# Kernel optimization log

Measured on AMD Instinct MI355X. Metric: run time of the kernel, lower is better.

The kernel has to match this reference:

```python
import jax, jax.numpy as jnp
import numpy as np

DIM = 512
HEADS = 8
DIM_HEAD = 64
INNER = HEADS * DIM_HEAD          # 512
GROUPS = 8                        # offset_groups
OFF_D = INNER // GROUPS           # 64
DS = 4                            # downsample_factor
KS = 6                            # offset_kernel_size
OFF_SCALE = 4.0                   # offset_scale (defaults to downsample_factor)
SCALE = DIM_HEAD ** -0.5


def conv1d(x, w, b=None, stride=1, padding=0, groups=1):
    # x: (B, Cin, N), w: (Cout, Cin//groups, K)
    out = jax.lax.conv_general_dilated(
        x, w, (stride,), [(padding, padding)],
        dimension_numbers=('NCH', 'OIH', 'NCH'), feature_group_count=groups)
    if b is not None:
        out = out + b[None, :, None]
    return out


def grid_sample_1d(feats, grid):
    # Faithful to F.grid_sample(mode='bilinear', padding_mode='zeros', align_corners=False)
    # applied along a length-N axis (the 2D workaround's width dim is size 1 -> identity).
    # feats: (B, C, N), grid: (B, M) normalized coords.
    N = feats.shape[-1]
    pos = ((grid + 1.0) * N - 1.0) * 0.5          # unnormalize, align_corners=False
    x0 = jnp.floor(pos)
    w1 = (pos - x0)[:, None, :]                    # fractional weight, (B,1,M)

    def gather(idx):
        valid = ((idx >= 0) & (idx < N))[:, None, :]
        idxc = jnp.clip(idx, 0, N - 1).astype(jnp.int32)
        g = jnp.take_along_axis(feats, idxc[:, None, :], axis=2)  # (B,C,M)
        return g * valid

    return gather(x0) * (1.0 - w1) + gather(x0 + 1.0) * w1


def setup_inputs() -> dict:
    key = jax.random.key(0)
    ks = jax.random.split(key, 10)
    n = 4096
    x = jax.random.normal(ks[0], (1, n, DIM), dtype=jnp.float32)
    prev_x = jax.random.normal(ks[1], (1, n, DIM), dtype=jnp.float32)

    def w(k, shape, fan_in):
        return jax.random.normal(k, shape, dtype=jnp.float32) * (fan_in ** -0.5)

    Wq = w(ks[2], (INNER, 2 * DIM // GROUPS, 1), 2 * DIM // GROUPS)   # grouped 1x1
    Wk = w(ks[3], (INNER, DIM // GROUPS, 1), DIM // GROUPS)
    Wv = w(ks[4], (INNER, DIM // GROUPS, 1), DIM // GROUPS)
    Wo = w(ks[5], (DIM, INNER, 1), INNER)
    bo = jnp.zeros((DIM,), dtype=jnp.float32)
    Woff_dw = w(ks[6], (OFF_D, 1, KS), KS)                             # depthwise
    boff_dw = jnp.zeros((OFF_D,), dtype=jnp.float32)
    Woff_p = w(ks[7], (1, OFF_D, 1), OFF_D)                            # to 1 channel
    return {"x": x, "prev_x": prev_x, "Wq": Wq, "Wk": Wk, "Wv": Wv,
            "Wo": Wo, "bo": bo, "Woff_dw": Woff_dw, "boff_dw": boff_dw,
            "Woff_p": Woff_p}


def reference(x, prev_x, Wq, Wk, Wv, Wo, bo, Woff_dw, boff_dw, Woff_p):
    b = x.shape[0]                    # must be 1 (module's einsum relies on broadcast)
    x_t = jnp.swapaxes(x, 1, 2)       # (b, dim, n)
    px_t = jnp.swapaxes(prev_x, 1, 2)
    n = x_t.shape[-1]

    cq = jnp.concatenate([px_t, x_t], axis=1)          # (b, 2*dim, n)
    q = conv1d(cq, Wq, groups=GROUPS)                  # (b, inner, n)

    # offset network on grouped queries
    gq = q.reshape(b * GROUPS, OFF_D, n)
    h = conv1d(gq, Woff_dw, boff_dw, stride=DS, padding=(KS - DS) // 2, groups=OFF_D)
    h = jax.nn.gelu(h, approximate=False)
    off = conv1d(h, Woff_p)[:, 0, :]                   # (b*g, m)
    off = jnp.tanh(off) * OFF_SCALE
    m = off.shape[-1]                                  # n // DS

    vgrid = jnp.arange(m, dtype=off.dtype) + off       # (b*g, m)
    vgrid = 2.0 * vgrid / max(m - 1, 1) - 1.0          # normalize_grid
    vgrid = jnp.tile(vgrid, (2, 1))                    # (2*b*g, m)

    kv_in = jnp.concatenate([px_t, x_t], axis=0)       # (2b, dim, n)
    gkv = kv_in.reshape(2 * b * GROUPS, OFF_D, n)
    kv = grid_sample_1d(gkv, vgrid)                    # (2bg, off_d, m)
    kv = kv.reshape(2 * b, INNER, m)

    k = conv1d(kv, Wk, groups=GROUPS)                  # (2b, inner, m)
    v = conv1d(kv, Wv, groups=GROUPS)

    qh = (q * SCALE).reshape(b, HEADS, DIM_HEAD, n).transpose(0, 1, 3, 2)   # (b,h,n,d)
    kh = k.reshape(2 * b, HEADS, DIM_HEAD, m).transpose(0, 1, 3, 2)         # (2b,h,m,d)
    vh = v.reshape(2 * b, HEADS, DIM_HEAD, m).transpose(0, 1, 3, 2)

    qh = jnp.broadcast_to(qh, (2 * b,) + qh.shape[1:])  # explicit torch-einsum broadcast
    sim = jnp.einsum('bhid,bhjd->bhij', qh, kh)         # (2b,h,n,m)
    attn = jax.nn.softmax(sim, axis=-1)
    out = jnp.einsum('bhij,bhjd->bhid', attn, vh)       # (2b,h,n,d)

    out = out.transpose(0, 1, 3, 2).reshape(2 * b, INNER, n)
    out = conv1d(out, Wo, bo)                           # (2b, dim, n)
    out = jnp.swapaxes(out, 1, 2)                       # (2b, n, dim)
    out = out.reshape(2, b, n, DIM)
    return out.mean(axis=0)                             # (b, n, dim) -- avg prev/cur streams
```

## Files before the change

kernel.cpp:

```cpp
#include <hip/hip_runtime.h>
#include <math.h>

#define DIMC 512
#define NG 8
#define QSCALE 0.18033688011112042f
#define MSHIFT 7.2134752044448170f

typedef _Float16 half8 __attribute__((ext_vector_type(8)));
typedef __fp16 fp16x2 __attribute__((ext_vector_type(2)));
typedef float f32x4 __attribute__((ext_vector_type(4)));

__device__ __forceinline__ half8 frag_f32(const float* p) {
    float4 a = *(const float4*)p;
    float4 b = *(const float4*)(p + 4);
    union { fp16x2 h2[4]; half8 h8; } u;
    u.h2[0] = __builtin_amdgcn_cvt_pkrtz(a.x, a.y);
    u.h2[1] = __builtin_amdgcn_cvt_pkrtz(a.z, a.w);
    u.h2[2] = __builtin_amdgcn_cvt_pkrtz(b.x, b.y);
    u.h2[3] = __builtin_amdgcn_cvt_pkrtz(b.z, b.w);
    return u.h8;
}

__global__ __launch_bounds__(256, 2) void k_front(
    const float* __restrict__ x, const float* __restrict__ px,
    const float* __restrict__ Wq, const float* __restrict__ Wk,
    const float* __restrict__ Wv, const float* __restrict__ Wo,
    const float* __restrict__ Wdw, const float* __restrict__ bdw,
    const float* __restrict__ Wp, _Float16* __restrict__ qh,
    _Float16* __restrict__ kt16, _Float16* __restrict__ vt16,
    _Float16* __restrict__ Woh, int n, int m)
{
    __shared__ float Os[64*69];
    __shared__ float hl[2][64];
    __shared__ float part[16][16];
    __shared__ int   x0s[16];
    __shared__ float w1s[16];
    __shared__ _Float16 kvs[2][16*72];
    int g  = blockIdx.x & 7;
    int jt = blockIdx.x >> 3;
    int P0 = jt*64, j0 = jt*16;
    int t  = threadIdx.x;
    int lane = t & 63, w = t >> 6;
    int l15 = lane & 15, quad = lane >> 4;
    const float* SRC = (g < 4) ? px : x;
    int cbase = (g & 3) * 128;

    if (blockIdx.x < 128) {
        int idx = blockIdx.x*2048 + t*8;
        float4 a = *(const float4*)&Wo[idx];
        float4 b = *(const float4*)&Wo[idx+4];
        union { fp16x2 h2[4]; uint4 v; } pk;
        pk.h2[0] = __builtin_amdgcn_cvt_pkrtz(a.x, a.y);
        pk.h2[1] = __builtin_amdgcn_cvt_pkrtz(a.z, a.w);
        pk.h2[2] = __builtin_amdgcn_cvt_pkrtz(b.x, b.y);
        pk.h2[3] = __builtin_amdgcn_cvt_pkrtz(b.z, b.w);
        *(uint4*)&Woh[idx] = pk.v;
    }

    if (t < 128) {
        int side = t >> 6, c = t & 63;
        int p = P0 + (side ? 64 : -1);
        float hsum = 0.f;
        if (p >= 0 && p < n) {
            const float* xr = &SRC[(size_t)p*DIMC + cbase];
            const float* wr = &Wq[(size_t)(g*64 + c)*128];
#pragma unroll 8
            for (int k = 0; k < 32; ++k) {
                float4 xv = *(const float4*)&xr[k*4];
                float4 wv = *(const float4*)&wr[k*4];
                hsum += xv.x*wv.x + xv.y*wv.y + xv.z*wv.z + xv.w*wv.w;
            }
        }
        hl[side][c] = hsum;
    }

    half8 af[4];
#pragma unroll
    for (int ks = 0; ks < 4; ++ks)
        af[ks] = frag_f32(&SRC[(size_t)(P0 + w*16 + l15)*DIMC + cbase + ks*32 + quad*8]);
    f32x4 acc[4];
#pragma unroll
    for (int nt = 0; nt < 4; ++nt) acc[nt] = (f32x4){0.f,0.f,0.f,0.f};
#pragma unroll
    for (int ks = 0; ks < 4; ++ks)
#pragma unroll
        for (int nt = 0; nt < 4; ++nt) {
            half8 bf = frag_f32(&Wq[(size_t)(g*64 + nt*16 + l15)*128 + ks*32 + quad*8]);
            acc[nt] = __builtin_amdgcn_mfma_f32_16x16x32_f16(af[ks], bf, acc[nt], 0, 0, 0);
        }
#pragma unroll
    for (int nt = 0; nt < 4; ++nt)
#pragma unroll
        for (int r = 0; r < 4; ++r)
            Os[(w*16 + quad*4 + r)*69 + nt*16 + l15] = acc[nt][r];
    __syncthreads();

    {
        int i = t >> 2, hf = t & 3;
        union { _Float16 h[16]; uint4 v[2]; } pk;
#pragma unroll
        for (int u = 0; u < 16; ++u) pk.h[u] = (_Float16)(Os[i*69 + hf*16 + u] * QSCALE);
        uint4* dst = (uint4*)&qh[((size_t)g*n + P0 + i)*64 + hf*16];
        dst[0] = pk.v[0]; dst[1] = pk.v[1];
    }

    {
        int j = t & 15, cg = t >> 4;
        float acco = 0.f;
#pragma unroll
        for (int cc = 0; cc < 4; ++cc) {
            int c = cg*4 + cc;
            float h = bdw[c];
#pragma unroll
            for (int tt = 0; tt < 6; ++tt) {
                int lp = 4*j + tt - 1;
                float val = (lp < 0) ? hl[0][c] : (lp >= 64 ? hl[1][c] : Os[lp*69 + c]);
                h += Wdw[c*6 + tt] * val;
            }
            float ge = 0.5f * h * (1.0f + erff(h * 0.70710678118654752f));
            acco += Wp[c] * ge;
        }
        part[cg][j] = acco;
    }
    __syncthreads();
    if (t < 16) {
        float off = 0.f;
#pragma unroll
        for (int cg2 = 0; cg2 < 16; ++cg2) off += part[cg2][t];
        off = tanhf(off) * 4.0f;
        int jg = j0 + t;
        float vg  = 2.0f * ((float)jg + off) / (float)(m - 1) - 1.0f;
        float pos = ((vg + 1.0f) * (float)n - 1.0f) * 0.5f;
        float x0  = floorf(pos);
        x0s[t] = (int)x0;
        w1s[t] = pos - x0;
    }
    __syncthreads();

    {
        float a0[4], a1[4], b0[4], b1[4], wg[4];
#pragma unroll
        for (int jj = 0; jj < 4; ++jj) {
            int j = jj*4 + w;
            int ii = x0s[j];
            wg[jj] = w1s[j];
            bool v0 = (ii   >= 0 && ii   < n);
            bool v1 = (ii+1 >= 0 && ii+1 < n);
            a0[jj] = v0 ? px[(size_t)ii*DIMC + g*64 + lane]     : 0.f;
            a1[jj] = v1 ? px[(size_t)(ii+1)*DIMC + g*64 + lane] : 0.f;
            b0[jj] = v0 ? x[(size_t)ii*DIMC + g*64 + lane]      : 0.f;
            b1[jj] = v1 ? x[(size_t)(ii+1)*DIMC + g*64 + lane]  : 0.f;
        }
#pragma unroll
        for (int jj = 0; jj < 4; ++jj) {
            kvs[0][(jj*4 + w)*72 + lane] = (_Float16)(a0[jj]*(1.0f - wg[jj]) + a1[jj]*wg[jj]);
            kvs[1][(jj*4 + w)*72 + lane] = (_Float16)(b0[jj]*(1.0f - wg[jj]) + b1[jj]*wg[jj]);
        }
    }
    __syncthreads();

    half8 bk[2], bv[2];
#pragma unroll
    for (int ks = 0; ks < 2; ++ks) {
        bk[ks] = frag_f32(&Wk[(size_t)(g*64 + w*16 + l15)*64 + ks*32 + quad*8]);
        bv[ks] = frag_f32(&Wv[(size_t)(g*64 + w*16 + l15)*64 + ks*32 + quad*8]);
    }
#pragma unroll
    for (int s = 0; s < 2; ++s) {
        half8 afk[2];
#pragma unroll
        for (int ks = 0; ks < 2; ++ks)
            afk[ks] = *(const half8*)&kvs[s][l15*72 + ks*32 + quad*8];
        f32x4 ack = (f32x4){0.f,0.f,0.f,0.f};
        f32x4 acv = (f32x4){0.f,0.f,0.f,0.f};
#pragma unroll
        for (int ks = 0; ks < 2; ++ks) {
            ack = __builtin_amdgcn_mfma_f32_16x16x32_f16(afk[ks], bk[ks], ack, 0, 0, 0);
            acv = __builtin_amdgcn_mfma_f32_16x16x32_f16(afk[ks], bv[ks], acv, 0, 0, 0);
        }
        size_t hb = (size_t)(s*8 + g);
#pragma unroll
        for (int r = 0; r < 4; ++r)
            kt16[(hb*m + j0 + quad*4 + r)*64 + w*16 + l15] = (_Float16)ack[r];
        union { fp16x2 h2[2]; uint2 v; } pv;
        pv.h2[0] = __builtin_amdgcn_cvt_pkrtz(acv[0], acv[1]);
        pv.h2[1] = __builtin_amdgcn_cvt_pkrtz(acv[2], acv[3]);
        *(uint2*)&vt16[(hb*64 + w*16 + l15)*m + j0 + quad*4] = pv.v;
    }
}

__global__ __launch_bounds__(256, 2) void k_attn(
    const _Float16* __restrict__ qh, const _Float16* __restrict__ kt16,
    const _Float16* __restrict__ vt16, _Float16* __restrict__ aoh, int n, int m)
{
    __shared__ _Float16 Vs[2][64*72];
    __shared__ _Float16 Ps[128*72];
    int nit = n >> 7;
    int it = blockIdx.x % nit;
    int h  = (blockIdx.x / nit) & 7;
    int s  = blockIdx.x / (nit*8);
    int t  = threadIdx.x;
    int lane = t & 63, w = t >> 6;
    int l15 = lane & 15, quad = lane >> 4;
    int i0 = it*128;

    const _Float16* qb = &qh[((size_t)h*n + i0)*64];
    half8 bqv[2][2];
#pragma unroll
    for (int ks = 0; ks < 2; ++ks)
#pragma unroll
        for (int i2 = 0; i2 < 2; ++i2)
            bqv[ks][i2] = *(const half8*)&qb[(w*32 + i2*16 + l15)*64 + ks*32 + quad*8];

    const _Float16* kb = &kt16[(size_t)(s*8+h)*m*64];
    const _Float16* vb = &vt16[(size_t)(s*8+h)*64*m];

    int r0 = t >> 3, oct = t & 7;

    float lsum[2] = {0.f, 0.f};
    f32x4 oaccT[4][2];
#pragma unroll
    for (int dt = 0; dt < 4; ++dt)
#pragma unroll
        for (int i2 = 0; i2 < 2; ++i2) oaccT[dt][i2] = (f32x4){0.f,0.f,0.f,0.f};

    uint4 pv0 = *(const uint4*)&vb[(size_t)r0*m + oct*8];
    uint4 pv1 = *(const uint4*)&vb[(size_t)(r0+32)*m + oct*8];
    *(uint4*)&Vs[0][r0*72 + oct*8]      = pv0;
    *(uint4*)&Vs[0][(r0+32)*72 + oct*8] = pv1;

    int ntile = m >> 6;
    for (int tk = 0; tk < ntile; ++tk) {
        bool pf = (tk + 1 < ntile);
        if (pf) {
            pv0 = *(const uint4*)&vb[(size_t)r0*m + (tk+1)*64 + oct*8];
            pv1 = *(const uint4*)&vb[(size_t)(r0+32)*m + (tk+1)*64 + oct*8];
        }
        half8 aqv[2][4];
#pragma unroll
        for (int ks = 0; ks < 2; ++ks)
#pragma unroll
            for (int jt = 0; jt < 4; ++jt)
                aqv[ks][jt] = *(const half8*)&kb[(size_t)(tk*64 + jt*16 + l15)*64 + ks*32 + quad*8];

        __syncthreads();
        const _Float16* VB = Vs[tk & 1];
        half8 avv[2][4];
#pragma unroll
        for (int ks = 0; ks < 2; ++ks)
#pragma unroll
            for (int dt = 0; dt < 4; ++dt)
                avv[ks][dt] = *(const half8*)&VB[(dt*16 + l15)*72 + ks*32 + quad*8];

        f32x4 accs[4][2];
#pragma unroll
        for (int jt = 0; jt < 4; ++jt)
#pragma unroll
            for (int i2 = 0; i2 < 2; ++i2) accs[jt][i2] = (f32x4){0.f,0.f,0.f,0.f};
        __builtin_amdgcn_s_setprio(1);
#pragma unroll
        for (int ks = 0; ks < 2; ++ks)
#pragma unroll
            for (int jt = 0; jt < 4; ++jt)
#pragma unroll
                for (int i2 = 0; i2 < 2; ++i2)
                    accs[jt][i2] = __builtin_amdgcn_mfma_f32_16x16x32_f16(
                        aqv[ks][jt], bqv[ks][i2], accs[jt][i2], 0, 0, 0);
        __builtin_amdgcn_s_setprio(0);

#pragma unroll
        for (int jt = 0; jt < 4; ++jt)
#pragma unroll
            for (int i2 = 0; i2 < 2; ++i2) {
                f32x4 p;
#pragma unroll
                for (int r = 0; r < 4; ++r) p[r] = __builtin_amdgcn_exp2f(accs[jt][i2][r] - MSHIFT);
                lsum[i2] += (p[0]+p[1]) + (p[2]+p[3]);
                union { fp16x2 h; int i; } c0, c1;
                c0.h = __builtin_amdgcn_cvt_pkrtz(p[0], p[1]);
                c1.h = __builtin_amdgcn_cvt_pkrtz(p[2], p[3]);
                *(int2*)&Ps[(w*32 + i2*16 + l15)*72 + jt*16 + quad*4] = make_int2(c0.i, c1.i);
            }

        __builtin_amdgcn_s_setprio(1);
#pragma unroll
        for (int ks = 0; ks < 2; ++ks)
#pragma unroll
            for (int i2 = 0; i2 < 2; ++i2) {
                half8 bp = *(const half8*)&Ps[(w*32 + i2*16 + l15)*72 + ks*32 + quad*8];
#pragma unroll
                for (int dt = 0; dt < 4; ++dt)
                    oaccT[dt][i2] = __builtin_amdgcn_mfma_f32_16x16x32_f16(
                        avv[ks][dt], bp, oaccT[dt][i2], 0, 0, 0);
            }
        __builtin_amdgcn_s_setprio(0);

        if (pf) {
            int b2 = (tk + 1) & 1;
            *(uint4*)&Vs[b2][r0*72 + oct*8]      = pv0;
            *(uint4*)&Vs[b2][(r0+32)*72 + oct*8] = pv1;
        }
    }

#pragma unroll
    for (int i2 = 0; i2 < 2; ++i2) {
        lsum[i2] += __shfl_xor(lsum[i2], 16, 64);
        lsum[i2] += __shfl_xor(lsum[i2], 32, 64);
    }
    float inv[2] = {1.0f / lsum[0], 1.0f / lsum[1]};
#pragma unroll
    for (int dt = 0; dt < 4; ++dt)
#pragma unroll
        for (int i2 = 0; i2 < 2; ++i2)
#pragma unroll
            for (int r = 0; r < 4; ++r)
                Ps[(w*32 + i2*16 + l15)*72 + dt*16 + quad*4 + r]
                    = (_Float16)(oaccT[dt][i2][r] * inv[i2]);
    {
        int row = w*32 + (lane >> 1);
        int dbase = (lane & 1) * 32;
        size_t gbase = (size_t)(i0 + row)*1024 + s*512 + h*64 + dbase;
#pragma unroll
        for (int k2 = 0; k2 < 4; ++k2) {
            uint4 v = *(uint4*)&Ps[row*72 + dbase + k2*8];
            *(uint4*)&aoh[gbase + k2*8] = v;
        }
    }
}

__global__ __launch_bounds__(256) void k_out(
    const _Float16* __restrict__ aoh, const _Float16* __restrict__ Woh,
    const float* __restrict__ bo, float* __restrict__ out, int n)
{
    int i0 = blockIdx.x*64, d0 = blockIdx.y*64;
    int t = threadIdx.x;
    int lane = t & 63, w = t >> 6;
    int l15 = lane & 15, quad = lane >> 4;
    f32x4 oacc[4];
#pragma unroll
    for (int dt = 0; dt < 4; ++dt) oacc[dt] = (f32x4){0.f,0.f,0.f,0.f};

    const _Float16* arow = &aoh[(size_t)(i0 + w*16 + l15)*1024 + quad*8];
#pragma unroll 4
    for (int ks = 0; ks < 16; ++ks) {
        half8 aq0 = *(const half8*)&arow[ks*32];
        half8 aq1 = *(const half8*)&arow[(ks+16)*32];
        half8 aqs = aq0 + aq1;
        int cbase = ks * 32;
#pragma unroll
        for (int dt = 0; dt < 4; ++dt) {
            half8 bw = *(const half8*)&Woh[(size_t)(d0 + dt*16 + l15)*DIMC + cbase + quad*8];
            oacc[dt] = __builtin_amdgcn_mfma_f32_16x16x32_f16(aqs, bw, oacc[dt], 0, 0, 0);
        }
    }
#pragma unroll
    for (int dt = 0; dt < 4; ++dt) {
        float bias = bo[d0 + dt*16 + l15];
#pragma unroll
        for (int r = 0; r < 4; ++r)
            out[(size_t)(i0 + w*16 + quad*4 + r)*DIMC + d0 + dt*16 + l15]
                = bias + 0.5f*oacc[dt][r];
    }
}

extern "C" void kernel_launch(void* const* d_in, const int* in_sizes, int n_in,
                              void* d_out, int out_size, void* d_ws, size_t ws_size,
                              hipStream_t stream)
{
    const float* x   = (const float*)d_in[0];
    const float* px  = (const float*)d_in[1];
    const float* Wq  = (const float*)d_in[2];
    const float* Wk  = (const float*)d_in[3];
    const float* Wv  = (const float*)d_in[4];
    const float* Wo  = (const float*)d_in[5];
    const float* bo  = (const float*)d_in[6];
    const float* Wdw = (const float*)d_in[7];
    const float* bdw = (const float*)d_in[8];
    const float* Wp  = (const float*)d_in[9];
    float* out = (float*)d_out;
    int n = in_sizes[0] / DIMC;
    int m = n / 4;

    _Float16* qhf  = (_Float16*)d_ws;
    _Float16* kt16 = qhf + (size_t)8*n*64;
    _Float16* vt16 = kt16 + (size_t)16*m*64;
    _Float16* aoh  = vt16 + (size_t)16*m*64;
    _Float16* Woh  = aoh + (size_t)n*1024;

    k_front<<<8*(m/16),    256, 0, stream>>>(x, px, Wq, Wk, Wv, Wo, Wdw, bdw, Wp,
                                             qhf, kt16, vt16, Woh, n, m);
    k_attn <<<2*8*(n/128), 256, 0, stream>>>(qhf, kt16, vt16, aoh, n, m);
    k_out  <<<dim3(n/64, 8), 256, 0, stream>>>(aoh, Woh, bo, out, n);
}
```

Measured before the change: 158.1 us.

## Load V fragments directly from global into registers, drop shared-memory staging

The attention kernel no longer stages V tiles through a double-buffered shared-memory array with a per-tile __syncthreads. Each wave now loads its V MFMA fragments straight from global memory into registers, ping-ponging two register sets across an unrolled-by-two loop so the next tile's load overlaps the current tile's compute. This removes the block barrier and the shared-memory round trip. In exchange it raises register pressure, and the global reads are strided by m per row instead of being issued cooperatively and coalesced. Each wave also re-reads the full V tile rather than sharing one copy.

Result: slower. 185.0 us (+17.0%).

```diff
diff --git a/kernel.cpp b/kernel.cpp
--- a/kernel.cpp
+++ b/kernel.cpp
@@ -189,11 +189,83 @@
     }
 }
 
+struct AttnCtx {
+    const _Float16* kb;
+    const _Float16* vb;
+    _Float16* Ps;
+    int m, w, l15, quad;
+};
+
+__device__ __forceinline__ void load_v(const AttnCtx& c, half8 (&dst)[2][4], int tk) {
+#pragma unroll
+    for (int ks = 0; ks < 2; ++ks)
+#pragma unroll
+        for (int dt = 0; dt < 4; ++dt)
+            dst[ks][dt] = *(const half8*)&c.vb[(size_t)(dt*16 + c.l15)*c.m
+                                              + tk*64 + ks*32 + c.quad*8];
+}
+
+__device__ __forceinline__ void attn_body(
+    const AttnCtx& c, int tk, const half8 (&avv)[2][4],
+    const half8 (&bqv)[2][2], float (&lsum)[2], f32x4 (&oaccT)[4][2])
+{
+    half8 aqv[2][4];
+#pragma unroll
+    for (int ks = 0; ks < 2; ++ks)
+#pragma unroll
+        for (int jt = 0; jt < 4; ++jt)
+            aqv[ks][jt] = *(const half8*)&c.kb[(size_t)(tk*64 + jt*16 + c.l15)*64
+                                              + ks*32 + c.quad*8];
+
+    f32x4 accs[4][2];
+#pragma unroll
+    for (int jt = 0; jt < 4; ++jt)
+#pragma unroll
+        for (int i2 = 0; i2 < 2; ++i2) accs[jt][i2] = (f32x4){0.f,0.f,0.f,0.f};
+    __builtin_amdgcn_s_setprio(1);
+#pragma unroll
+    for (int ks = 0; ks < 2; ++ks)
+#pragma unroll
+        for (int jt = 0; jt < 4; ++jt)
+#pragma unroll
+            for (int i2 = 0; i2 < 2; ++i2)
+                accs[jt][i2] = __builtin_amdgcn_mfma_f32_16x16x32_f16(
+                    aqv[ks][jt], bqv[ks][i2], accs[jt][i2], 0, 0, 0);
+    __builtin_amdgcn_s_setprio(0);
+
+#pragma unroll
+    for (int jt = 0; jt < 4; ++jt)
+#pragma unroll
+        for (int i2 = 0; i2 < 2; ++i2) {
+            f32x4 p;
+#pragma unroll
+            for (int r = 0; r < 4; ++r) p[r] = __builtin_amdgcn_exp2f(accs[jt][i2][r] - MSHIFT);
+            lsum[i2] += (p[0]+p[1]) + (p[2]+p[3]);
+            union { fp16x2 h; int i; } c0, c1;
+            c0.h = __builtin_amdgcn_cvt_pkrtz(p[0], p[1]);
+            c1.h = __builtin_amdgcn_cvt_pkrtz(p[2], p[3]);
+            *(int2*)&c.Ps[(c.w*32 + i2*16 + c.l15)*72 + jt*16 + c.quad*4]
+                = make_int2(c0.i, c1.i);
+        }
+
+    __builtin_amdgcn_s_setprio(1);
+#pragma unroll
+    for (int ks = 0; ks < 2; ++ks)
+#pragma unroll
+        for (int i2 = 0; i2 < 2; ++i2) {
+            half8 bp = *(const half8*)&c.Ps[(c.w*32 + i2*16 + c.l15)*72 + ks*32 + c.quad*8];
+#pragma unroll
+            for (int dt = 0; dt < 4; ++dt)
+                oaccT[dt][i2] = __builtin_amdgcn_mfma_f32_16x16x32_f16(
+                    avv[ks][dt], bp, oaccT[dt][i2], 0, 0, 0);
+        }
+    __builtin_amdgcn_s_setprio(0);
+}
+
 __global__ __launch_bounds__(256, 2) void k_attn(
     const _Float16* __restrict__ qh, const _Float16* __restrict__ kt16,
     const _Float16* __restrict__ vt16, _Float16* __restrict__ aoh, int n, int m)
 {
-    __shared__ _Float16 Vs[2][64*72];
     __shared__ _Float16 Ps[128*72];
     int nit = n >> 7;
     int it = blockIdx.x % nit;
@@ -212,10 +284,10 @@
         for (int i2 = 0; i2 < 2; ++i2)
             bqv[ks][i2] = *(const half8*)&qb[(w*32 + i2*16 + l15)*64 + ks*32 + quad*8];
 
-    const _Float16* kb = &kt16[(size_t)(s*8+h)*m*64];
-    const _Float16* vb = &vt16[(size_t)(s*8+h)*64*m];
-
-    int r0 = t >> 3, oct = t & 7;
+    AttnCtx c;
+    c.kb = &kt16[(size_t)(s*8+h)*m*64];
+    c.vb = &vt16[(size_t)(s*8+h)*64*m];
+    c.Ps = Ps; c.m = m; c.w = w; c.l15 = l15; c.quad = quad;
 
     float lsum[2] = {0.f, 0.f};
     f32x4 oaccT[4][2];
@@ -224,81 +296,16 @@
 #pragma unroll
         for (int i2 = 0; i2 < 2; ++i2) oaccT[dt][i2] = (f32x4){0.f,0.f,0.f,0.f};
 
-    uint4 pv0 = *(const uint4*)&vb[(size_t)r0*m + oct*8];
-    uint4 pv1 = *(const uint4*)&vb[(size_t)(r0+32)*m + oct*8];
-    *(uint4*)&Vs[0][r0*72 + oct*8]      = pv0;
-    *(uint4*)&Vs[0][(r0+32)*72 + oct*8] = pv1;
+    half8 avvA[2][4], avvB[2][4];
+    load_v(c, avvA, 0);
 
     int ntile = m >> 6;
-    for (int tk = 0; tk < ntile; ++tk) {
-        bool pf = (tk + 1 < ntile);
-        if (pf) {
-            pv0 = *(const uint4*)&vb[(size_t)r0*m + (tk+1)*64 + oct*8];
-            pv1 = *(const uint4*)&vb[(size_t)(r0+32)*m + (tk+1)*64 + oct*8];
-        }
-        half8 aqv[2][4];
-#pragma unroll
-        for (int ks = 0; ks < 2; ++ks)
-#pragma unroll
-            for (int jt = 0; jt < 4; ++jt)
-                aqv[ks][jt] = *(const half8*)&kb[(size_t)(tk*64 + jt*16 + l15)*64 + ks*32 + quad*8];
-
-        __syncthreads();
-        const _Float16* VB = Vs[tk & 1];
-        half8 avv[2][4];
-#pragma unroll
-        for (int ks = 0; ks < 2; ++ks)
-#pragma unroll
-            for (int dt = 0; dt < 4; ++dt)
-                avv[ks][dt] = *(const half8*)&VB[(dt*16 + l15)*72 + ks*32 + quad*8];
-
-        f32x4 accs[4][2];
-#pragma unroll
-        for (int jt = 0; jt < 4; ++jt)
-#pragma unroll
-            for (int i2 = 0; i2 < 2; ++i2) accs[jt][i2] = (f32x4){0.f,0.f,0.f,0.f};
-        __builtin_amdgcn_s_setprio(1);
-#pragma unroll
-        for (int ks = 0; ks < 2; ++ks)
-#pragma unroll
-            for (int jt = 0; jt < 4; ++jt)
-#pragma unroll
-                for (int i2 = 0; i2 < 2; ++i2)
-                    accs[jt][i2] = __builtin_amdgcn_mfma_f32_16x16x32_f16(
-                        aqv[ks][jt], bqv[ks][i2], accs[jt][i2], 0, 0, 0);
-        __builtin_amdgcn_s_setprio(0);
-
-#pragma unroll
-        for (int jt = 0; jt < 4; ++jt)
-#pragma unroll
-            for (int i2 = 0; i2 < 2; ++i2) {
-                f32x4 p;
-#pragma unroll
-                for (int r = 0; r < 4; ++r) p[r] = __builtin_amdgcn_exp2f(accs[jt][i2][r] - MSHIFT);
-                lsum[i2] += (p[0]+p[1]) + (p[2]+p[3]);
-                union { fp16x2 h; int i; } c0, c1;
-                c0.h = __builtin_amdgcn_cvt_pkrtz(p[0], p[1]);
-                c1.h = __builtin_amdgcn_cvt_pkrtz(p[2], p[3]);
-                *(int2*)&Ps[(w*32 + i2*16 + l15)*72 + jt*16 + quad*4] = make_int2(c0.i, c1.i);
-            }
-
-        __builtin_amdgcn_s_setprio(1);
-#pragma unroll
-        for (int ks = 0; ks < 2; ++ks)
-#pragma unroll
-            for (int i2 = 0; i2 < 2; ++i2) {
-                half8 bp = *(const half8*)&Ps[(w*32 + i2*16 + l15)*72 + ks*32 + quad*8];
-#pragma unroll
-                for (int dt = 0; dt < 4; ++dt)
-                    oaccT[dt][i2] = __builtin_amdgcn_mfma_f32_16x16x32_f16(
-                        avv[ks][dt], bp, oaccT[dt][i2], 0, 0, 0);
-            }
-        __builtin_amdgcn_s_setprio(0);
-
-        if (pf) {
-            int b2 = (tk + 1) & 1;
-            *(uint4*)&Vs[b2][r0*72 + oct*8]      = pv0;
-            *(uint4*)&Vs[b2][(r0+32)*72 + oct*8] = pv1;
+    for (int tk = 0; tk < ntile; tk += 2) {
+        if (tk + 1 < ntile) load_v(c, avvB, tk + 1);
+        attn_body(c, tk, avvA, bqv, lsum, oaccT);
+        if (tk + 1 < ntile) {
+            if (tk + 2 < ntile) load_v(c, avvA, tk + 2);
+            attn_body(c, tk + 1, avvB, bqv, lsum, oaccT);
         }
     }
 
```
